# Kernel tuning notes

Hardware: AMD Instinct MI355X
Metric: run time of the kernel (lower is better)

The kernel has to match this reference:

```python
import jax, jax.numpy as jnp
import numpy as np

LOG2 = float(np.log(2.0))

def ssp(x):
    # shifted softplus, the PhysNet-family activation: softplus(x) - ln(2)
    return jax.nn.softplus(x) - LOG2

def setup_inputs() -> dict:
    key = jax.random.key(0)
    k1, k2, k3, k4, k5 = jax.random.split(key, 5)
    N, E, D_EDGE, D_RBF = 50000, 640000, 128, 64
    vi = jax.random.normal(k1, (N, D_EDGE), dtype=jnp.float32)
    rbf = jax.random.uniform(k2, (E, D_RBF), dtype=jnp.float32)
    edge_index = jax.random.randint(k3, (2, E), 0, N, dtype=jnp.int64)
    # torch.nn.Linear params: y = x @ W.T + b, W ~ U(-1/sqrt(fan_in), 1/sqrt(fan_in))
    s1 = 1.0 / np.sqrt(D_RBF)
    s2 = 1.0 / np.sqrt(3 * D_EDGE)
    W_rbf = jax.random.uniform(k4, (D_EDGE, D_RBF), jnp.float32, -s1, s1)
    b_rbf = jnp.zeros((D_EDGE,), jnp.float32)
    W_cat = jax.random.uniform(k5, (D_EDGE, 3 * D_EDGE), jnp.float32, -s2, s2)
    b_cat = jnp.zeros((D_EDGE,), jnp.float32)
    return {"vi": vi, "rbf": rbf, "W_rbf": W_rbf, "b_rbf": b_rbf,
            "W_cat": W_cat, "b_cat": b_cat, "edge_index": edge_index}

def reference(vi, rbf, W_rbf, b_rbf, W_cat, b_cat, edge_index):
    # gather endpoint features per edge: [E, D]
    h_i = vi[edge_index[0], :]
    h_j = vi[edge_index[1], :]
    rbf_proj = rbf @ W_rbf.T + b_rbf              # [E, D]
    concat_msg = jnp.concatenate([rbf_proj, h_j, h_i], axis=-1)  # [E, 3D]
    m_ji = ssp(concat_msg @ W_cat.T + b_cat)      # [E, D]
    return m_ji
```

## Files before the change

### kernel.cpp

```cpp
#include <hip/hip_runtime.h>
#include <cmath>

#define D  128
#define DR 64
#define NB 32

typedef float fx4    __attribute__((ext_vector_type(4)));
typedef float f32x16 __attribute__((ext_vector_type(16)));
typedef short short8v __attribute__((ext_vector_type(8)));

__device__ __forceinline__ float ssp_f(float x) {
  float m = fmaxf(x, 0.0f);
  float t = __expf(-fabsf(x));
  return m + __logf(1.0f + t) - 0.69314718055994531f;
}

__device__ __forceinline__ short f2bf(float f) {
  unsigned u = __float_as_uint(f);
  u = (u + 0x7FFFu + ((u >> 16) & 1u)) >> 16;
  return (short)u;
}

__device__ __forceinline__ float bf2f(unsigned short h) {
  return __uint_as_float(((unsigned)h) << 16);
}

__global__ __launch_bounds__(256) void prep_kernel(
    const float* __restrict__ vi, const float* __restrict__ W_cat,
    const float* __restrict__ W_rbf, const float* __restrict__ b_rbf,
    const float* __restrict__ b_cat,
    unsigned short* __restrict__ PjH, unsigned short* __restrict__ PiH,
    float* __restrict__ weff, unsigned short* __restrict__ weffh,
    float* __restrict__ beff, int N, int nb1, int write_bf16)
{
  const int t = threadIdx.x;
  if (blockIdx.x >= nb1) {
    int gid = (blockIdx.x - nb1) * 256 + t;
    if (gid < D * DR) {
      int o = gid >> 6;
      int r = gid & 63;
      float acc = 0.0f;
      #pragma unroll 8
      for (int d = 0; d < D; ++d)
        acc = fmaf(W_cat[o * 384 + d], W_rbf[d * DR + r], acc);
      weff[gid] = acc;
      if (write_bf16) weffh[gid] = (unsigned short)f2bf(acc);
    }
    if (gid < D) {
      float acc = b_cat[gid];
      #pragma unroll 8
      for (int d = 0; d < D; ++d)
        acc = fmaf(b_rbf[d], W_cat[gid * 384 + d], acc);
      beff[gid] = acc;
    }
    return;
  }

  __shared__ float vrow[NB * D];
  int base = blockIdx.x * NB;
  for (int idx = t * 4; idx < NB * D; idx += 1024) {
    int n = base + (idx >> 7);
    float4 v = make_float4(0.f, 0.f, 0.f, 0.f);
    if (n < N) v = *(const float4*)&vi[(long)n * D + (idx & 127)];
    *(float4*)&vrow[idx] = v;
  }
  __syncthreads();

  int o     = t & 127;
  int which = t >> 7;
  const float* w = W_cat + (long)o * 384 + 128 + which * 128;
  unsigned short* P = which ? PiH : PjH;

  float acc[NB];
  #pragma unroll
  for (int n = 0; n < NB; ++n) acc[n] = 0.0f;

  for (int dd = 0; dd < D; dd += 4) {
    float4 wv = *(const float4*)&w[dd];
    #pragma unroll
    for (int n = 0; n < NB; ++n) {
      float4 v = *(const float4*)&vrow[n * D + dd];
      acc[n] = fmaf(wv.x, v.x, acc[n]);
      acc[n] = fmaf(wv.y, v.y, acc[n]);
      acc[n] = fmaf(wv.z, v.z, acc[n]);
      acc[n] = fmaf(wv.w, v.w, acc[n]);
    }
  }
  #pragma unroll
  for (int n = 0; n < NB; ++n) {
    int nn = base + n;
    if (nn < N) P[(long)nn * D + o] = (unsigned short)f2bf(acc[n]);
  }
}

__global__ __launch_bounds__(64) void edge_mfma_kernel(
    const float* __restrict__ rbf, const int* __restrict__ eidx,
    const unsigned short* __restrict__ weffh, const float* __restrict__ beff,
    const unsigned short* __restrict__ PjH, const unsigned short* __restrict__ PiH,
    float* __restrict__ out, int E)
{
  const int lane = threadIdx.x & 63;
  const int row  = lane & 31;
  const int half = lane >> 5;
  const long base = (long)blockIdx.x * 64;
  if (base >= (long)E) return;

  short8v B[4][4];
  #pragma unroll
  for (int ct = 0; ct < 4; ++ct) {
    #pragma unroll
    for (int ks = 0; ks < 4; ++ks)
      B[ct][ks] = *(const short8v*)&weffh[(ct * 32 + row) * DR + ks * 16 + half * 8];
  }
  float bias[4];
  #pragma unroll
  for (int ct = 0; ct < 4; ++ct) bias[ct] = beff[ct * 32 + row];

  #pragma unroll
  for (int tile = 0; tile < 2; ++tile) {
    const long tb = base + (long)tile * 32;
    if (tb >= (long)E) break;
    long er = tb + row; if (er > (long)E - 1) er = (long)E - 1;

    const float* arow = rbf + er * DR + half * 8;
    short8v A[4];
    #pragma unroll
    for (int ks = 0; ks < 4; ++ks) {
      fx4 lo = __builtin_nontemporal_load((const fx4*)&arow[ks * 16]);
      fx4 hi = __builtin_nontemporal_load((const fx4*)&arow[ks * 16 + 4]);
      short8v a;
      a[0] = f2bf(lo.x); a[1] = f2bf(lo.y); a[2] = f2bf(lo.z); a[3] = f2bf(lo.w);
      a[4] = f2bf(hi.x); a[5] = f2bf(hi.y); a[6] = f2bf(hi.z); a[7] = f2bf(hi.w);
      A[ks] = a;
    }

    const int iv = eidx[er];
    const int jv = eidx[(long)E + er];

    #pragma unroll
    for (int ct = 0; ct < 4; ++ct) {
      float gj[16], gi[16];
      #pragma unroll
      for (int reg = 0; reg < 16; ++reg) {
        const int erl = (reg & 3) + 8 * (reg >> 2) + 4 * half;
        const int j = __shfl(jv, erl);
        const int i = __shfl(iv, erl);
        gj[reg] = bf2f(PjH[(long)j * D + ct * 32 + row]);
        gi[reg] = bf2f(PiH[(long)i * D + ct * 32 + row]);
      }
      __builtin_amdgcn_sched_barrier(0);

      f32x16 acc = (f32x16)(0.0f);
      acc = __builtin_amdgcn_mfma_f32_32x32x16_bf16(A[0], B[ct][0], acc, 0, 0, 0);
      acc = __builtin_amdgcn_mfma_f32_32x32x16_bf16(A[1], B[ct][1], acc, 0, 0, 0);
      acc = __builtin_amdgcn_mfma_f32_32x32x16_bf16(A[2], B[ct][2], acc, 0, 0, 0);
      acc = __builtin_amdgcn_mfma_f32_32x32x16_bf16(A[3], B[ct][3], acc, 0, 0, 0);

      #pragma unroll
      for (int reg = 0; reg < 16; ++reg) {
        const int erl = (reg & 3) + 8 * (reg >> 2) + 4 * half;
        const long ge = tb + erl;
        const float v = ssp_f(acc[reg] + gj[reg] + gi[reg] + bias[ct]);
        if (ge < (long)E)
          __builtin_nontemporal_store(v, &out[ge * D + ct * 32 + row]);
      }
    }
  }
}

template<int K, int WS, int WOFF, bool GATHER, bool INIT, bool FINAL>
__global__ __launch_bounds__(256) void pass_kernel(
    const float* __restrict__ src, const int* __restrict__ gidx,
    const float* __restrict__ W, const float* __restrict__ beff,
    float* __restrict__ out, int E)
{
  int e = blockIdx.x * 256 + threadIdx.x;
  if (e >= E) return;
  long rowi = GATHER ? (long)gidx[e] : (long)e;

  float4 rv[K / 4];
  const float4* sp = (const float4*)(src + rowi * K);
  #pragma unroll
  for (int c = 0; c < K / 4; ++c) rv[c] = sp[c];

  float* orow = out + (long)e * D;
  for (int ob = 0; ob < D; ob += 4) {
    float acc[4];
    if (INIT) {
      float4 b4 = *(const float4*)&beff[ob];
      acc[0] = b4.x; acc[1] = b4.y; acc[2] = b4.z; acc[3] = b4.w;
    } else {
      float4 p4 = *(const float4*)&orow[ob];
      acc[0] = p4.x; acc[1] = p4.y; acc[2] = p4.z; acc[3] = p4.w;
    }
    #pragma unroll
    for (int k = 0; k < 4; ++k) {
      const float4* wv = (const float4*)&W[(long)(ob + k) * WS + WOFF];
      float a = acc[k];
      #pragma unroll
      for (int c = 0; c < K / 4; ++c) {
        float4 w4 = wv[c]; float4 r4 = rv[c];
        a = fmaf(w4.x, r4.x, a); a = fmaf(w4.y, r4.y, a);
        a = fmaf(w4.z, r4.z, a); a = fmaf(w4.w, r4.w, a);
      }
      acc[k] = a;
    }
    float4 o4;
    o4.x = FINAL ? ssp_f(acc[0]) : acc[0];
    o4.y = FINAL ? ssp_f(acc[1]) : acc[1];
    o4.z = FINAL ? ssp_f(acc[2]) : acc[2];
    o4.w = FINAL ? ssp_f(acc[3]) : acc[3];
    *(float4*)&orow[ob] = o4;
  }
}

extern "C" void kernel_launch(void* const* d_in, const int* in_sizes, int n_in,
                              void* d_out, int out_size, void* d_ws, size_t ws_size,
                              hipStream_t stream)
{
  const float* vi    = (const float*)d_in[0];
  const float* rbf   = (const float*)d_in[1];
  const float* W_rbf = (const float*)d_in[2];
  const float* b_rbf = (const float*)d_in[3];
  const float* W_cat = (const float*)d_in[4];
  const float* b_cat = (const float*)d_in[5];
  const int*   eidx  = (const int*)d_in[6];

  const int N = in_sizes[0] / D;
  const int E = in_sizes[6] / 2;
  float* out = (float*)d_out;

  float* ws   = (float*)d_ws;
  float* weff = ws;
  float* beff = ws + D * DR;
  unsigned short* weffh = (unsigned short*)(ws + 8448);
  unsigned short* PjH = (unsigned short*)(ws + 8448 + 4096);
  unsigned short* PiH = PjH + (size_t)N * D;
  size_t need = (8448 + 4096 + (size_t)N * 128) * sizeof(float);

  const int use_fast = (ws_size >= need && E >= 1);

  if (use_fast) {
    int nb1 = (N + NB - 1) / NB;
    prep_kernel<<<nb1 + 32, 256, 0, stream>>>(vi, W_cat, W_rbf, b_rbf, b_cat,
                                              PjH, PiH, weff, weffh, beff,
                                              N, nb1, 1);
    int fblocks = (int)(((long)E + 63) / 64);
    edge_mfma_kernel<<<fblocks, 64, 0, stream>>>(rbf, eidx, weffh, beff,
                                                 PjH, PiH, out, E);
  } else {
    prep_kernel<<<32, 256, 0, stream>>>(vi, W_cat, W_rbf, b_rbf, b_cat,
                                        PjH, PiH, weff, weffh, beff,
                                        N, 0, 0);
    int eblocks = (E + 255) / 256;
    pass_kernel<DR, DR, 0,  false, true,  false><<<eblocks, 256, 0, stream>>>(rbf, nullptr,  weff,  beff, out, E);
    pass_kernel<D, 384, 128, true, false, false><<<eblocks, 256, 0, stream>>>(vi,  eidx + E, W_cat, beff, out, E);
    pass_kernel<D, 384, 256, true, false, true ><<<eblocks, 256, 0, stream>>>(vi,  eidx,     W_cat, beff, out, E);
  }
}
```

Measured before the change: 275.2 us.

## Compute node projections in prep kernel with bf16 MFMA instead of scalar FMA

```diff
diff --git a/kernel.cpp b/kernel.cpp
--- a/kernel.cpp
+++ b/kernel.cpp
@@ -3,7 +3,6 @@
 
 #define D  128
 #define DR 64
-#define NB 32
 
 typedef float fx4    __attribute__((ext_vector_type(4)));
 typedef float f32x16 __attribute__((ext_vector_type(16)));
@@ -23,6 +22,15 @@
 
 __device__ __forceinline__ float bf2f(unsigned short h) {
   return __uint_as_float(((unsigned)h) << 16);
+}
+
+__device__ __forceinline__ short8v cvt8(const float* p) {
+  fx4 lo = *(const fx4*)p;
+  fx4 hi = *(const fx4*)(p + 4);
+  short8v r;
+  r[0] = f2bf(lo.x); r[1] = f2bf(lo.y); r[2] = f2bf(lo.z); r[3] = f2bf(lo.w);
+  r[4] = f2bf(hi.x); r[5] = f2bf(hi.y); r[6] = f2bf(hi.z); r[7] = f2bf(hi.w);
+  return r;
 }
 
 __global__ __launch_bounds__(256) void prep_kernel(
@@ -31,11 +39,11 @@
     const float* __restrict__ b_cat,
     unsigned short* __restrict__ PjH, unsigned short* __restrict__ PiH,
     float* __restrict__ weff, unsigned short* __restrict__ weffh,
-    float* __restrict__ beff, int N, int nb1, int write_bf16)
+    float* __restrict__ beff, int N, int nbt, int write_bf16)
 {
   const int t = threadIdx.x;
-  if (blockIdx.x >= nb1) {
-    int gid = (blockIdx.x - nb1) * 256 + t;
+  if ((int)blockIdx.x >= nbt) {
+    int gid = ((int)blockIdx.x - nbt) * 256 + t;
     if (gid < D * DR) {
       int o = gid >> 6;
       int r = gid & 63;
@@ -56,40 +64,48 @@
     return;
   }
 
-  __shared__ float vrow[NB * D];
-  int base = blockIdx.x * NB;
-  for (int idx = t * 4; idx < NB * D; idx += 1024) {
-    int n = base + (idx >> 7);
-    float4 v = make_float4(0.f, 0.f, 0.f, 0.f);
-    if (n < N) v = *(const float4*)&vi[(long)n * D + (idx & 127)];
-    *(float4*)&vrow[idx] = v;
-  }
-  __syncthreads();
-
-  int o     = t & 127;
-  int which = t >> 7;
-  const float* w = W_cat + (long)o * 384 + 128 + which * 128;
-  unsigned short* P = which ? PiH : PjH;
-
-  float acc[NB];
-  #pragma unroll
-  for (int n = 0; n < NB; ++n) acc[n] = 0.0f;
-
-  for (int dd = 0; dd < D; dd += 4) {
-    float4 wv = *(const float4*)&w[dd];
-    #pragma unroll
-    for (int n = 0; n < NB; ++n) {
-      float4 v = *(const float4*)&vrow[n * D + dd];
-      acc[n] = fmaf(wv.x, v.x, acc[n]);
-      acc[n] = fmaf(wv.y, v.y, acc[n]);
-      acc[n] = fmaf(wv.z, v.z, acc[n]);
-      acc[n] = fmaf(wv.w, v.w, acc[n]);
-    }
-  }
-  #pragma unroll
-  for (int n = 0; n < NB; ++n) {
-    int nn = base + n;
-    if (nn < N) P[(long)nn * D + o] = (unsigned short)f2bf(acc[n]);
+  const int lane = t & 63;
+  const int col  = lane & 31;
+  const int half = lane >> 5;
+  const long wid  = (long)blockIdx.x * 4 + (t >> 6);
+  const long base = wid * 64;
+  if (base >= (long)N) return;
+
+  #pragma unroll
+  for (int tile = 0; tile < 2; ++tile) {
+    const long tb = base + (long)tile * 32;
+    if (tb >= (long)N) break;
+    long nr = tb + col; if (nr > (long)N - 1) nr = (long)N - 1;
+
+    const float* arow = vi + nr * D + half * 8;
+    short8v A[8];
+    #pragma unroll
+    for (int ks = 0; ks < 8; ++ks)
+      A[ks] = cvt8(&arow[ks * 16]);
+
+    #pragma unroll
+    for (int ct = 0; ct < 8; ++ct) {
+      const int off = 128 + (ct >> 2) * 128;
+      const int o   = (ct & 3) * 32 + col;
+      const float* wrow = W_cat + (long)o * 384 + off + half * 8;
+
+      f32x16 acc = (f32x16)(0.0f);
+      #pragma unroll
+      for (int ks = 0; ks < 8; ++ks) {
+        short8v Bv = cvt8(&wrow[ks * 16]);
+        acc = __builtin_amdgcn_mfma_f32_32x32x16_bf16(A[ks], Bv, acc, 0, 0, 0);
+      }
+
+      unsigned short* P = (ct < 4) ? PjH : PiH;
+      const int cb = (ct & 3) * 32;
+      #pragma unroll
+      for (int reg = 0; reg < 16; ++reg) {
+        const int erl = (reg & 3) + 8 * (reg >> 2) + 4 * half;
+        const long nn = tb + erl;
+        if (nn < (long)N)
+          P[nn * D + cb + col] = (unsigned short)f2bf(acc[reg]);
+      }
+    }
   }
 }
 
@@ -241,10 +257,11 @@
   const int use_fast = (ws_size >= need && E >= 1);
 
   if (use_fast) {
-    int nb1 = (N + NB - 1) / NB;
-    prep_kernel<<<nb1 + 32, 256, 0, stream>>>(vi, W_cat, W_rbf, b_rbf, b_cat,
+    long twaves = ((long)N + 63) / 64;
+    int nbt = (int)((twaves + 3) / 4);
+    prep_kernel<<<nbt + 32, 256, 0, stream>>>(vi, W_cat, W_rbf, b_rbf, b_cat,
                                               PjH, PiH, weff, weffh, beff,
-                                              N, nb1, 1);
+                                              N, nbt, 1);
     int fblocks = (int)(((long)E + 63) / 64);
     edge_mfma_kernel<<<fblocks, 64, 0, stream>>>(rbf, eidx, weffh, beff,
                                                  PjH, PiH, out, E);
```

Measured after the change: 245.9 us, median of 2. 1.12x faster.
